# Kernel optimization log

Hardware: AMD Instinct MI355X
Metric: run time of the kernel (lower is better)

The kernel has to match this reference:

```python
import jax, jax.numpy as jnp
import numpy as np

B, S, C = 32, 1024, 12      # sentences, words per sentence, chars per word
E, H = 256, 512             # embedding dim, word-LSTM hidden dim
V, CS, T = 50000, 128, 50   # vocab, charset, tagset


def _lstm(x, Wih, Whh, b):
    """Standard torch LSTM (gate order i,f,g,o). x: [T, N, I] -> hidden trace [T, N, H]."""
    Hd = Whh.shape[1]
    N = x.shape[1]
    h0 = jnp.zeros((N, Hd), x.dtype)
    c0 = jnp.zeros((N, Hd), x.dtype)

    def step(carry, xt):
        h, c = carry
        gates = xt @ Wih.T + h @ Whh.T + b
        i, f, g, o = jnp.split(gates, 4, axis=-1)
        c = jax.nn.sigmoid(f) * c + jax.nn.sigmoid(i) * jnp.tanh(g)
        h = jax.nn.sigmoid(o) * jnp.tanh(c)
        return (h, c), h

    _, hs = jax.lax.scan(step, (h0, c0), x)
    return hs


def setup_inputs() -> dict:
    key = jax.random.key(0)
    ks = jax.random.split(key, 12)
    sc = 0.05
    return {
        "char_idx": jax.random.randint(ks[0], (B, S, C), 0, CS),
        "word_idx": jax.random.randint(ks[1], (B, S), 0, V),
        "char_emb": jax.random.normal(ks[2], (CS, E), jnp.float32) * sc,
        "word_emb": jax.random.normal(ks[3], (V, E), jnp.float32) * sc,
        "Wc_ih": jax.random.normal(ks[4], (4 * E, E), jnp.float32) * sc,
        "Wc_hh": jax.random.normal(ks[5], (4 * E, E), jnp.float32) * sc,
        "bc": jnp.zeros((4 * E,), jnp.float32),
        "Ww_ih": jax.random.normal(ks[6], (4 * H, 2 * E), jnp.float32) * sc,
        "Ww_hh": jax.random.normal(ks[7], (4 * H, H), jnp.float32) * sc,
        "bw": jnp.zeros((4 * H,), jnp.float32),
        "Wt": jax.random.normal(ks[8], (T, H), jnp.float32) * sc,
        "bt": jnp.zeros((T,), jnp.float32),
    }


def reference(char_idx, word_idx, char_emb, word_emb, Wc_ih, Wc_hh, bc,
              Ww_ih, Ww_hh, bw, Wt, bt):
    # --- character-level LSTM: each word starts from a fresh zero state ---
    ce = char_emb[char_idx]                       # [B, S, C, E]
    ce = ce.reshape(B * S, C, E).transpose(1, 0, 2)  # [C, B*S, E]
    char_hs = _lstm(ce, Wc_ih, Wc_hh, bc)         # [C, B*S, E]
    char_feat = char_hs[-1].reshape(B, S, E)      # last char output per word

    # --- word-level LSTM over concatenated [word_emb ; char_feat] ---
    we = word_emb[word_idx]                       # [B, S, E]
    x = jnp.concatenate([we, char_feat], axis=-1) # [B, S, 2E]
    x = x.transpose(1, 0, 2)                      # [S, B, 2E]
    word_hs = _lstm(x, Ww_ih, Ww_hh, bw)          # [S, B, H]
    word_hs = word_hs.transpose(1, 0, 2)          # [B, S, H]

    # --- tag projection + log_softmax per token ---
    logits = word_hs @ Wt.T + bt                  # [B, S, T]
    return jax.nn.log_softmax(logits, axis=-1)
```

## Files before the change

### kernel.cpp

```cpp
#include <hip/hip_runtime.h>
#include <stdint.h>
#include <stddef.h>

#define NB   32
#define NS   1024
#define NC   12
#define NE   256
#define NH   512
#define NT   50
#define NWRD 32768
#define MC   1024
#define RW   2048
#define KW   512

typedef short bf16x8 __attribute__((ext_vector_type(8)));
typedef short bf16x4 __attribute__((ext_vector_type(4)));
typedef float f32x4  __attribute__((ext_vector_type(4)));

#define MFMA16(a,b,c) __builtin_amdgcn_mfma_f32_16x16x32_bf16(a, b, c, 0, 0, 0)

__device__ __forceinline__ float bf2f(short u){
  return __uint_as_float(((uint32_t)(uint16_t)u) << 16);
}
__device__ __forceinline__ short f2bf(float f){
  uint32_t u = __float_as_uint(f);
  uint32_t r = (u + 0x7FFFu + ((u >> 16) & 1u)) >> 16;
  return (short)r;
}
__device__ __forceinline__ float sigf(float x){
  float e = __expf(-fabsf(x));
  float s = 1.0f / (1.0f + e);
  return x >= 0.0f ? s : 1.0f - s;
}
__device__ __forceinline__ float tanh_f(float x){
  float e = __expf(-2.0f * fabsf(x));
  float r = (1.0f - e) / (1.0f + e);
  return x >= 0.0f ? r : -r;
}

__global__ __launch_bounds__(256) void k_prep_pe(
    const float* __restrict__ char_emb, const float* __restrict__ Wc_ih,
    const float* __restrict__ bc, float* __restrict__ PEb)
{
  __shared__ float ce[NE];
  int a = blockIdx.x, tid = threadIdx.x;
  ce[tid] = char_emb[a * NE + tid];
  __syncthreads();
  int j = tid;
  float acc[4];
  #pragma unroll
  for (int g = 0; g < 4; ++g) acc[g] = 0.0f;
  for (int k = 0; k < NE; ++k) {
    float c = ce[k];
    #pragma unroll
    for (int g = 0; g < 4; ++g)
      acc[g] += c * Wc_ih[(size_t)(g * NE + j) * NE + k];
  }
  float4 o;
  o.x = acc[0] + bc[0 * NE + j];
  o.y = acc[1] + bc[1 * NE + j];
  o.z = acc[2] + bc[2 * NE + j];
  o.w = acc[3] + bc[3 * NE + j];
  *(float4*)&PEb[(size_t)a * MC + j * 4] = o;
}

__global__ __launch_bounds__(256) void k_prep_w(
    const float* __restrict__ Wc_hh, const float* __restrict__ Ww_ih,
    const float* __restrict__ Ww_hh, const float* __restrict__ bw,
    short* __restrict__ WhhC, short* __restrict__ WihW,
    short* __restrict__ WhhW, float* __restrict__ bwI)
{
  int r = blockIdx.x;
  int j = r >> 2, g = r & 3, tid = threadIdx.x;
  if (r < MC) {
    float v = Wc_hh[(size_t)(g * NE + j) * NE + tid];
    WhhC[(size_t)r * NE + tid] = f2bf(v);
  }
  #pragma unroll
  for (int kk = 0; kk < 2; ++kk) {
    int k = tid + kk * 256;
    WihW[(size_t)r * KW + k] = f2bf(Ww_ih[(size_t)(g * NH + j) * KW + k]);
    WhhW[(size_t)r * NH + k] = f2bf(Ww_hh[(size_t)(g * NH + j) * NH + k]);
  }
  if (tid == 0) bwI[r] = bw[g * NH + j];
}

__global__ __launch_bounds__(256) void k_char0(
    const int* __restrict__ char_idx, const float* __restrict__ PEb,
    float* __restrict__ c_state, short* __restrict__ h_out)
{
  int w = blockIdx.x, j = threadIdx.x;
  int idx = char_idx[w * NC + 0];
  float4 pe = *(const float4*)&PEb[(size_t)idx * MC + j * 4];
  float c = sigf(pe.x) * tanh_f(pe.z);
  float h = sigf(pe.w) * tanh_f(c);
  c_state[(size_t)w * NE + j] = c;
  h_out[(size_t)w * NE + j] = f2bf(h);
}

template<int KDIM, int EPI>
__global__ __launch_bounds__(256) void gemm_epi(
    const short* __restrict__ Amat, const short* __restrict__ Bmat,
    const float* __restrict__ PEb, const int* __restrict__ char_idx, int tstep,
    float* __restrict__ c_state, short* __restrict__ h_out,
    const float* __restrict__ bias, short* __restrict__ pw_out)
{
  __shared__ __align__(16) short As[128 * 64];
  __shared__ __align__(16) short Bs[128 * 64];
  const int tid = threadIdx.x;
  const int lane = tid & 63;
  const int wid = tid >> 6;
  const int wm = wid >> 1, wn = wid & 1;
  const int m0 = blockIdx.y * 128;
  const int n0 = blockIdx.x * 128;
  const int lo = lane & 15, hi = lane >> 4;

  f32x4 acc[4][4];
  #pragma unroll
  for (int i = 0; i < 4; ++i)
    #pragma unroll
    for (int j = 0; j < 4; ++j) acc[i][j] = (f32x4)0.0f;

  const int nk = KDIM / 64;
  for (int ki = 0; ki < nk; ++ki) {
    __syncthreads();
    #pragma unroll
    for (int it = 0; it < 4; ++it) {
      int cid = tid + it * 256;
      int row = cid >> 3, cp = cid & 7;
      int kch = cp ^ (row & 7);
      *(bf16x8*)&As[row * 64 + cp * 8] =
          *(const bf16x8*)&Amat[(size_t)(m0 + row) * KDIM + ki * 64 + kch * 8];
      *(bf16x8*)&Bs[row * 64 + cp * 8] =
          *(const bf16x8*)&Bmat[(size_t)(n0 + row) * KDIM + ki * 64 + kch * 8];
    }
    __syncthreads();
    #pragma unroll
    for (int kc = 0; kc < 2; ++kc) {
      bf16x8 af[4], bfr[4];
      #pragma unroll
      for (int fm = 0; fm < 4; ++fm) {
        int row = wm * 64 + fm * 16 + lo;
        int ch = (kc * 4 + hi) ^ (row & 7);
        af[fm] = *(bf16x8*)&As[row * 64 + ch * 8];
      }
      #pragma unroll
      for (int fn = 0; fn < 4; ++fn) {
        int row = wn * 64 + fn * 16 + lo;
        int ch = (kc * 4 + hi) ^ (row & 7);
        bfr[fn] = *(bf16x8*)&Bs[row * 64 + ch * 8];
      }
      #pragma unroll
      for (int fm = 0; fm < 4; ++fm)
        #pragma unroll
        for (int fn = 0; fn < 4; ++fn)
          acc[fm][fn] = MFMA16(af[fm], bfr[fn], acc[fm][fn]);
    }
  }

  #pragma unroll
  for (int fm = 0; fm < 4; ++fm) {
    int r0 = m0 + wm * 64 + fm * 16 + hi * 4;
    #pragma unroll
    for (int fn = 0; fn < 4; ++fn) {
      int w = n0 + wn * 64 + fn * 16 + lo;
      if constexpr (EPI == 0) {
        int idx = char_idx[w * NC + tstep];
        float4 pe = *(const float4*)&PEb[(size_t)idx * MC + r0];
        float gi = acc[fm][fn][0] + pe.x;
        float gf = acc[fm][fn][1] + pe.y;
        float gg = acc[fm][fn][2] + pe.z;
        float go = acc[fm][fn][3] + pe.w;
        int j = r0 >> 2;
        float c = sigf(gf) * c_state[(size_t)w * NE + j] + sigf(gi) * tanh_f(gg);
        c_state[(size_t)w * NE + j] = c;
        h_out[(size_t)w * NE + j] = f2bf(sigf(go) * tanh_f(c));
      } else {
        float4 bb = *(const float4*)&bias[r0];
        bf16x4 o;
        o[0] = f2bf(acc[fm][fn][0] + bb.x);
        o[1] = f2bf(acc[fm][fn][1] + bb.y);
        o[2] = f2bf(acc[fm][fn][2] + bb.z);
        o[3] = f2bf(acc[fm][fn][3] + bb.w);
        *(bf16x4*)&pw_out[(size_t)w * RW + r0] = o;
      }
    }
  }
}

__global__ __launch_bounds__(64) void k_xw(
    const int* __restrict__ word_idx, const float* __restrict__ word_emb,
    const short* __restrict__ h_char, short* __restrict__ Xw)
{
  int wp = blockIdx.x;
  int s = wp >> 5, b = wp & 31;
  int w = b * NS + s;
  int tid = threadIdx.x;
  int widx = word_idx[w];
  #pragma unroll
  for (int g = 0; g < 2; ++g) {
    int k4 = (tid + g * 64) * 4;
    bf16x4 o;
    if (k4 < NE) {
      float4 v = *(const float4*)&word_emb[(size_t)widx * NE + k4];
      o[0] = f2bf(v.x); o[1] = f2bf(v.y); o[2] = f2bf(v.z); o[3] = f2bf(v.w);
    } else {
      o = *(const bf16x4*)&h_char[(size_t)w * NE + (k4 - NE)];
    }
    *(bf16x4*)&Xw[(size_t)wp * KW + k4] = o;
  }
}

__global__ __launch_bounds__(512, 2) void k_word(
    const short* __restrict__ Whh,
    const short* __restrict__ PW,
    unsigned long long* __restrict__ hx64,
    short* __restrict__ word_hs)
{
  __shared__ __align__(16) short h_lds[2][32 * 520];
  const int tid = threadIdx.x, lane = tid & 63, wv = tid >> 6;
  const int lo = lane & 15, hi = lane >> 4;
  const int bk = blockIdx.x;
  const int wr = wv >> 1, wc = wv & 1;
  const int rowbase = bk * 64 + wr * 16;
  const int b = wc * 16 + lo;
  const int jl = (rowbase >> 2) + hi;
  const int r4 = rowbase + hi * 4;

  bf16x8 a[16];
  #pragma unroll
  for (int kc = 0; kc < 16; ++kc)
    a[kc] = *(const bf16x8*)&Whh[(size_t)(rowbase + lo) * NH + kc * 32 + hi * 8];

  float cst = 0.0f;
  bf16x4 pw = *(const bf16x4*)&PW[(size_t)(0 * NB + b) * RW + r4];

  const int jp_own = tid & 255;
  const int bgrp = tid >> 8;

  for (int s = 0; s < NS; ++s) {
    int sn = (s + 1 < NS) ? (s + 1) : (NS - 1);
    bf16x4 pwn = *(const bf16x4*)&PW[(size_t)(sn * NB + b) * RW + r4];

    const unsigned long long* src = hx64 + ((s & 1) << 13);
    unsigned long long v[16];
    #pragma unroll
    for (int i = 0; i < 16; ++i)
      v[i] = __hip_atomic_load(&src[i * 512 + tid], __ATOMIC_RELAXED, __HIP_MEMORY_SCOPE_AGENT);
    const unsigned int tv = (unsigned int)s;
    for (;;) {
      bool ok = true;
      #pragma unroll
      for (int i = 0; i < 16; ++i) {
        if ((unsigned int)(v[i] >> 32) != tv) {
          ok = false;
          v[i] = __hip_atomic_load(&src[i * 512 + tid], __ATOMIC_RELAXED, __HIP_MEMORY_SCOPE_AGENT);
        }
      }
      if (ok) break;
      __builtin_amdgcn_s_sleep(1);
    }

    short* buf = &h_lds[s & 1][0];
    #pragma unroll
    for (int i = 0; i < 16; ++i) {
      int bb = 2 * i + bgrp;
      *(unsigned int*)&buf[bb * 520 + 2 * jp_own] = (unsigned int)v[i];
    }
    __syncthreads();

    f32x4 acc;
    #pragma unroll
    for (int q = 0; q < 4; ++q) acc[q] = bf2f(pw[q]);
    #pragma unroll
    for (int kc = 0; kc < 16; ++kc) {
      bf16x8 hb = *(bf16x8*)((const char*)buf + b * 1040 + kc * 64 + hi * 16);
      acc = MFMA16(a[kc], hb, acc);
    }

    float c = sigf(acc[1]) * cst + sigf(acc[0]) * tanh_f(acc[2]);
    cst = c;
    short hv = f2bf(sigf(acc[3]) * tanh_f(c));

    unsigned int own = (unsigned int)(unsigned short)hv;
    unsigned int part = (unsigned int)__shfl_xor((int)own, 16);
    if ((hi & 1) == 0) {
      unsigned long long val = (((unsigned long long)(unsigned int)(s + 1)) << 32)
                             | ((unsigned long long)part << 16) | (unsigned long long)own;
      __hip_atomic_store(&hx64[(((s + 1) & 1) << 13) + (b << 8) + (jl >> 1)], val,
                         __ATOMIC_RELAXED, __HIP_MEMORY_SCOPE_AGENT);
    }
    word_hs[((size_t)b * NS + s) * NH + jl] = hv;
    pw = pwn;
  }
}

__global__ __launch_bounds__(256) void k_tags(
    const short* __restrict__ word_hs, const float* __restrict__ Wt,
    const float* __restrict__ bt, float* __restrict__ out)
{
  __shared__ __align__(16) short Ws[64 * 256];
  const int tid = threadIdx.x, lane = tid & 63, wid = tid >> 6;
  const int lo = lane & 15, hi = lane >> 4;
  const int n0 = blockIdx.x * 128;
  const int wb = n0 + wid * 32;

  f32x4 acc[4][2];
  #pragma unroll
  for (int fm = 0; fm < 4; ++fm)
    #pragma unroll
    for (int fn = 0; fn < 2; ++fn) acc[fm][fn] = (f32x4)0.0f;

  for (int half = 0; half < 2; ++half) {
    __syncthreads();
    for (int cid = tid; cid < 2048; cid += 256) {
      int row = cid >> 5, cp = cid & 31;
      int kch = cp ^ (row & 7);
      bf16x8 v;
      if (row < NT) {
        const float* src = &Wt[(size_t)row * KW + half * 256 + kch * 8];
        #pragma unroll
        for (int e = 0; e < 8; ++e) v[e] = f2bf(src[e]);
      } else v = (bf16x8)0;
      *(bf16x8*)&Ws[row * 256 + cp * 8] = v;
    }
    __syncthreads();
    #pragma unroll
    for (int kc = 0; kc < 8; ++kc) {
      bf16x8 bfr[2];
      #pragma unroll
      for (int fn = 0; fn < 2; ++fn) {
        int w = wb + fn * 16 + lo;
        bfr[fn] = *(const bf16x8*)&word_hs[(size_t)w * KW + half * 256 + kc * 32 + hi * 8];
      }
      #pragma unroll
      for (int fm = 0; fm < 4; ++fm) {
        int row = fm * 16 + lo;
        int ch = (kc * 4 + hi) ^ (row & 7);
        bf16x8 av = *(bf16x8*)&Ws[row * 256 + ch * 8];
        acc[fm][0] = MFMA16(av, bfr[0], acc[fm][0]);
        acc[fm][1] = MFMA16(av, bfr[1], acc[fm][1]);
      }
    }
  }

  #pragma unroll
  for (int fn = 0; fn < 2; ++fn) {
    int w = wb + fn * 16 + lo;
    float lg[16];
    float m = -1e30f;
    #pragma unroll
    for (int fm = 0; fm < 4; ++fm)
      #pragma unroll
      for (int q = 0; q < 4; ++q) {
        int tg = fm * 16 + hi * 4 + q;
        float bv = (tg < NT) ? bt[tg] : 0.0f;
        float v = acc[fm][fn][q] + bv;
        lg[fm * 4 + q] = v;
        if (tg < NT) m = fmaxf(m, v);
      }
    m = fmaxf(m, __shfl_xor(m, 16));
    m = fmaxf(m, __shfl_xor(m, 32));
    float s = 0.0f;
    #pragma unroll
    for (int fm = 0; fm < 4; ++fm)
      #pragma unroll
      for (int q = 0; q < 4; ++q) {
        int tg = fm * 16 + hi * 4 + q;
        if (tg < NT) s += __expf(lg[fm * 4 + q] - m);
      }
    s += __shfl_xor(s, 16);
    s += __shfl_xor(s, 32);
    float lz = m + __logf(s);
    #pragma unroll
    for (int fm = 0; fm < 4; ++fm)
      #pragma unroll
      for (int q = 0; q < 4; ++q) {
        int tg = fm * 16 + hi * 4 + q;
        if (tg < NT) out[(size_t)w * NT + tg] = lg[fm * 4 + q] - lz;
      }
  }
}

extern "C" void kernel_launch(void* const* d_in, const int* in_sizes, int n_in,
                              void* d_out, int out_size, void* d_ws, size_t ws_size,
                              hipStream_t stream) {
  const int*   char_idx = (const int*)  d_in[0];
  const int*   word_idx = (const int*)  d_in[1];
  const float* char_emb = (const float*)d_in[2];
  const float* word_emb = (const float*)d_in[3];
  const float* Wc_ih    = (const float*)d_in[4];
  const float* Wc_hh    = (const float*)d_in[5];
  const float* bc       = (const float*)d_in[6];
  const float* Ww_ih    = (const float*)d_in[7];
  const float* Ww_hh    = (const float*)d_in[8];
  const float* bw       = (const float*)d_in[9];
  const float* Wt       = (const float*)d_in[10];
  const float* bt       = (const float*)d_in[11];
  float* out = (float*)d_out;

  const size_t MB = 1ull << 20;
  uint8_t* w8 = (uint8_t*)d_ws;
  float* PEb   = (float*)(w8 + 0);
  short* WhhC  = (short*)(w8 + 512 * 1024);
  short* WihW  = (short*)(w8 + 1 * MB);
  short* WhhW  = (short*)(w8 + 3 * MB);
  float* bwI   = (float*)(w8 + 5 * MB);
  unsigned long long* hx64 = (unsigned long long*)(w8 + 5 * MB + 64 * 1024);
  short* hA    = (short*)(w8 + 6 * MB);
  short* hB    = (short*)(w8 + 22 * MB);
  short* whs   = (short*)(w8 + 6 * MB);
  float* cC    = (float*)(w8 + 38 * MB);
  short* Xw    = (short*)(w8 + 38 * MB);
  short* PW    = (short*)(w8 + 70 * MB);

  k_prep_pe<<<128, 256, 0, stream>>>(char_emb, Wc_ih, bc, PEb);
  k_prep_w<<<2048, 256, 0, stream>>>(Wc_hh, Ww_ih, Ww_hh, bw, WhhC, WihW, WhhW, bwI);

  k_char0<<<NWRD, 256, 0, stream>>>(char_idx, PEb, cC, hA);
  for (int t = 1; t < NC; ++t) {
    short* src = (t & 1) ? hA : hB;
    short* dst = (t & 1) ? hB : hA;
    gemm_epi<256, 0><<<dim3(256, 8), 256, 0, stream>>>(
        WhhC, src, PEb, char_idx, t, cC, dst, nullptr, nullptr);
  }

  k_xw<<<NWRD, 64, 0, stream>>>(word_idx, word_emb, hB, Xw);
  gemm_epi<512, 1><<<dim3(256, 16), 256, 0, stream>>>(
      WihW, Xw, nullptr, nullptr, 0, nullptr, nullptr, bwI, PW);

  hipMemsetAsync(hx64, 0, 128 * 1024, stream);
  k_word<<<32, 512, 0, stream>>>(WhhW, PW, hx64, whs);

  k_tags<<<256, 256, 0, stream>>>(whs, Wt, bt, out);
}
```

Measured before the change: 4.632 ms.

## Replace tagged 64-bit h exchange with data plus per-wave flag protocol in word LSTM

The word-LSTM cross-block exchange no longer packs a step tag into every 64-bit hidden-state word. Each wave now stores plain bf16 pairs, waits for its stores to drain, then publishes a per-wave step flag. Consumers poll 256 flags with one vectorized sc1 load and a ballot, then bulk-load the hidden state in 16-byte chunks. This halves exchange traffic and reduces per-thread polling work, but adds a store-drain wait and relies on sc1 cache semantics for ordering. Separately, the MFMA chain is split into four independent accumulators to shorten the dependency chain.

After: 4.423 ms. 1.05x faster.

```diff
diff --git a/kernel.cpp b/kernel.cpp
--- a/kernel.cpp
+++ b/kernel.cpp
@@ -16,6 +16,7 @@
 typedef short bf16x8 __attribute__((ext_vector_type(8)));
 typedef short bf16x4 __attribute__((ext_vector_type(4)));
 typedef float f32x4  __attribute__((ext_vector_type(4)));
+typedef unsigned int u32x4 __attribute__((ext_vector_type(4)));
 
 #define MFMA16(a,b,c) __builtin_amdgcn_mfma_f32_16x16x32_bf16(a, b, c, 0, 0, 0)
 
@@ -214,7 +215,7 @@
 __global__ __launch_bounds__(512, 2) void k_word(
     const short* __restrict__ Whh,
     const short* __restrict__ PW,
-    unsigned long long* __restrict__ hx64,
+    uint8_t* __restrict__ xb,
     short* __restrict__ word_hs)
 {
   __shared__ __align__(16) short h_lds[2][32 * 520];
@@ -232,51 +233,84 @@
   for (int kc = 0; kc < 16; ++kc)
     a[kc] = *(const bf16x8*)&Whh[(size_t)(rowbase + lo) * NH + kc * 32 + hi * 8];
 
+  short*    hdat  = (short*)xb;
+  uint32_t* flags = (uint32_t*)(xb + 65536);
+
+  const int db = tid >> 4, dlo = (tid & 15) * 8;
+  const short* dA = hdat + db * 512 + dlo;
+  const short* dB = dA + 16384;
+  const uint32_t* fA = flags + lane * 4;
+  const uint32_t* fB = fA + 256;
+
   float cst = 0.0f;
-  bf16x4 pw = *(const bf16x4*)&PW[(size_t)(0 * NB + b) * RW + r4];
-
-  const int jp_own = tid & 255;
-  const int bgrp = tid >> 8;
+  bf16x4 pw = *(const bf16x4*)&PW[(size_t)b * RW + r4];
 
   for (int s = 0; s < NS; ++s) {
+    const uint32_t tv = (uint32_t)s;
+    const int par = s & 1;
+
     int sn = (s + 1 < NS) ? (s + 1) : (NS - 1);
     bf16x4 pwn = *(const bf16x4*)&PW[(size_t)(sn * NB + b) * RW + r4];
 
-    const unsigned long long* src = hx64 + ((s & 1) << 13);
-    unsigned long long v[16];
-    #pragma unroll
-    for (int i = 0; i < 16; ++i)
-      v[i] = __hip_atomic_load(&src[i * 512 + tid], __ATOMIC_RELAXED, __HIP_MEMORY_SCOPE_AGENT);
-    const unsigned int tv = (unsigned int)s;
-    for (;;) {
-      bool ok = true;
-      #pragma unroll
-      for (int i = 0; i < 16; ++i) {
-        if ((unsigned int)(v[i] >> 32) != tv) {
-          ok = false;
-          v[i] = __hip_atomic_load(&src[i * 512 + tid], __ATOMIC_RELAXED, __HIP_MEMORY_SCOPE_AGENT);
+    {
+      const uint32_t* fp = par ? fB : fA;
+      int tries = 0;
+      for (;;) {
+        u32x4 f;
+        asm volatile("global_load_dwordx4 %0, %1, off sc1\n\t"
+                     "s_waitcnt vmcnt(0)"
+                     : "=v"(f) : "v"(fp));
+        bool ok = (f[0] == tv) & (f[1] == tv) & (f[2] == tv) & (f[3] == tv);
+        if (__ballot(ok) == ~0ull) break;
+        if (++tries > 768) {
+          uint32_t g0 = __hip_atomic_load(fp + 0, __ATOMIC_RELAXED, __HIP_MEMORY_SCOPE_AGENT);
+          uint32_t g1 = __hip_atomic_load(fp + 1, __ATOMIC_RELAXED, __HIP_MEMORY_SCOPE_AGENT);
+          uint32_t g2 = __hip_atomic_load(fp + 2, __ATOMIC_RELAXED, __HIP_MEMORY_SCOPE_AGENT);
+          uint32_t g3 = __hip_atomic_load(fp + 3, __ATOMIC_RELAXED, __HIP_MEMORY_SCOPE_AGENT);
+          bool ok2 = (g0 == tv) & (g1 == tv) & (g2 == tv) & (g3 == tv);
+          if (__ballot(ok2) == ~0ull) break;
+          tries = 0;
         }
-      }
-      if (ok) break;
-      __builtin_amdgcn_s_sleep(1);
-    }
-
-    short* buf = &h_lds[s & 1][0];
-    #pragma unroll
-    for (int i = 0; i < 16; ++i) {
-      int bb = 2 * i + bgrp;
-      *(unsigned int*)&buf[bb * 520 + 2 * jp_own] = (unsigned int)v[i];
-    }
+        __builtin_amdgcn_s_sleep(1);
+      }
+    }
+
+    const short* sp = par ? dB : dA;
+    bf16x8 d0, d1, d2, d3;
+    asm volatile("global_load_dwordx4 %0, %4, off sc1\n\t"
+                 "global_load_dwordx4 %1, %4, off offset:256 sc1\n\t"
+                 "global_load_dwordx4 %2, %4, off offset:512 sc1\n\t"
+                 "global_load_dwordx4 %3, %4, off offset:768 sc1\n\t"
+                 "s_waitcnt vmcnt(0)"
+                 : "=v"(d0), "=v"(d1), "=v"(d2), "=v"(d3) : "v"(sp));
+
+    short* buf = &h_lds[par][0];
+    short* dst = buf + db * 520 + dlo;
+    *(bf16x8*)&dst[0]   = d0;
+    *(bf16x8*)&dst[128] = d1;
+    *(bf16x8*)&dst[256] = d2;
+    *(bf16x8*)&dst[384] = d3;
     __syncthreads();
 
+    f32x4 acc0, acc1, acc2, acc3;
+    #pragma unroll
+    for (int q = 0; q < 4; ++q) {
+      acc0[q] = bf2f(pw[q]); acc1[q] = 0.0f; acc2[q] = 0.0f; acc3[q] = 0.0f;
+    }
+    #pragma unroll
+    for (int kc = 0; kc < 16; kc += 4) {
+      bf16x8 h0 = *(bf16x8*)((const char*)buf + b * 1040 + (kc + 0) * 64 + hi * 16);
+      bf16x8 h1 = *(bf16x8*)((const char*)buf + b * 1040 + (kc + 1) * 64 + hi * 16);
+      bf16x8 h2 = *(bf16x8*)((const char*)buf + b * 1040 + (kc + 2) * 64 + hi * 16);
+      bf16x8 h3 = *(bf16x8*)((const char*)buf + b * 1040 + (kc + 3) * 64 + hi * 16);
+      acc0 = MFMA16(a[kc + 0], h0, acc0);
+      acc1 = MFMA16(a[kc + 1], h1, acc1);
+      acc2 = MFMA16(a[kc + 2], h2, acc2);
+      acc3 = MFMA16(a[kc + 3], h3, acc3);
+    }
     f32x4 acc;
     #pragma unroll
-    for (int q = 0; q < 4; ++q) acc[q] = bf2f(pw[q]);
-    #pragma unroll
-    for (int kc = 0; kc < 16; ++kc) {
-      bf16x8 hb = *(bf16x8*)((const char*)buf + b * 1040 + kc * 64 + hi * 16);
-      acc = MFMA16(a[kc], hb, acc);
-    }
+    for (int q = 0; q < 4; ++q) acc[q] = (acc0[q] + acc1[q]) + (acc2[q] + acc3[q]);
 
     float c = sigf(acc[1]) * cst + sigf(acc[0]) * tanh_f(acc[2]);
     cst = c;
@@ -284,11 +318,17 @@
 
     unsigned int own = (unsigned int)(unsigned short)hv;
     unsigned int part = (unsigned int)__shfl_xor((int)own, 16);
+    const int npar = (s + 1) & 1;
     if ((hi & 1) == 0) {
-      unsigned long long val = (((unsigned long long)(unsigned int)(s + 1)) << 32)
-                             | ((unsigned long long)part << 16) | (unsigned long long)own;
-      __hip_atomic_store(&hx64[(((s + 1) & 1) << 13) + (b << 8) + (jl >> 1)], val,
-                         __ATOMIC_RELAXED, __HIP_MEMORY_SCOPE_AGENT);
+      unsigned int val = own | (part << 16);
+      short* hp = hdat + (npar << 14) + b * 512 + jl;
+      asm volatile("global_store_dword %0, %1, off sc1" :: "v"(hp), "v"(val) : "memory");
+    }
+    asm volatile("s_waitcnt vmcnt(0)" ::: "memory");
+    if (lane == 0) {
+      uint32_t* fq = flags + npar * 256 + bk * 8 + wv;
+      asm volatile("global_store_dword %0, %1, off sc1"
+                   :: "v"(fq), "v"((uint32_t)(s + 1)) : "memory");
     }
     word_hs[((size_t)b * NS + s) * NH + jl] = hv;
     pw = pwn;
@@ -406,7 +446,7 @@
   short* WihW  = (short*)(w8 + 1 * MB);
   short* WhhW  = (short*)(w8 + 3 * MB);
   float* bwI   = (float*)(w8 + 5 * MB);
-  unsigned long long* hx64 = (unsigned long long*)(w8 + 5 * MB + 64 * 1024);
+  uint8_t* xb  = (uint8_t*)(w8 + 5 * MB + 64 * 1024);
   short* hA    = (short*)(w8 + 6 * MB);
   short* hB    = (short*)(w8 + 22 * MB);
   short* whs   = (short*)(w8 + 6 * MB);
@@ -429,8 +469,8 @@
   gemm_epi<512, 1><<<dim3(256, 16), 256, 0, stream>>>(
       WihW, Xw, nullptr, nullptr, 0, nullptr, nullptr, bwI, PW);
 
-  hipMemsetAsync(hx64, 0, 128 * 1024, stream);
-  k_word<<<32, 512, 0, stream>>>(WhhW, PW, hx64, whs);
+  hipMemsetAsync(xb, 0, 64 * 1024 + 2048, stream);
+  k_word<<<32, 512, 0, stream>>>(WhhW, PW, xb, whs);
 
   k_tags<<<256, 256, 0, stream>>>(whs, Wt, bt, out);
 }
```

## Repack word-LSTM cross-block handoff as tagged 32-bit words with vector polling

Applied to the files above, without the earlier changes.

The cross-block exchange of hidden state in the persistent word-LSTM kernel is reworked. Each thread now publishes a single 32-bit word (16-bit step tag plus bf16 value) instead of shuffling lanes to form 64-bit tagged pairs. Consumers poll with inline-asm dwordx4 loads carrying sc1 cache bits, re-fetching only stale chunks. The change also splits the MFMA accumulation into four independent chains, prefetches the input projection two steps ahead, and drops the min-blocks launch bound. The aim is lower per-step synchronization latency on the serial 1024-step path, at the cost of relying on hand-written memory ordering and cache-bit semantics for correctness.

Result: slower. 7.079 ms (+52.8%).

```diff
diff --git a/kernel.cpp b/kernel.cpp
--- a/kernel.cpp
+++ b/kernel.cpp
@@ -16,6 +16,8 @@
 typedef short bf16x8 __attribute__((ext_vector_type(8)));
 typedef short bf16x4 __attribute__((ext_vector_type(4)));
 typedef float f32x4  __attribute__((ext_vector_type(4)));
+typedef unsigned int u32x2 __attribute__((ext_vector_type(2)));
+typedef unsigned int u32x4 __attribute__((ext_vector_type(4)));
 
 #define MFMA16(a,b,c) __builtin_amdgcn_mfma_f32_16x16x32_bf16(a, b, c, 0, 0, 0)
 
@@ -211,10 +213,10 @@
   }
 }
 
-__global__ __launch_bounds__(512, 2) void k_word(
+__global__ __launch_bounds__(512) void k_word(
     const short* __restrict__ Whh,
     const short* __restrict__ PW,
-    unsigned long long* __restrict__ hx64,
+    uint32_t* __restrict__ hx,
     short* __restrict__ word_hs)
 {
   __shared__ __align__(16) short h_lds[2][32 * 520];
@@ -232,66 +234,104 @@
   for (int kc = 0; kc < 16; ++kc)
     a[kc] = *(const bf16x8*)&Whh[(size_t)(rowbase + lo) * NH + kc * 32 + hi * 8];
 
+  const int db = tid >> 4, q0 = (tid & 15) * 4;
+  const uint32_t* pA = hx + db * 512 + q0;
+  const uint32_t* pB = pA + 16384;
+
   float cst = 0.0f;
-  bf16x4 pw = *(const bf16x4*)&PW[(size_t)(0 * NB + b) * RW + r4];
-
-  const int jp_own = tid & 255;
-  const int bgrp = tid >> 8;
+  bf16x4 pw  = *(const bf16x4*)&PW[(size_t)(0 * NB + b) * RW + r4];
+  bf16x4 pw1 = *(const bf16x4*)&PW[(size_t)(1 * NB + b) * RW + r4];
 
   for (int s = 0; s < NS; ++s) {
-    int sn = (s + 1 < NS) ? (s + 1) : (NS - 1);
-    bf16x4 pwn = *(const bf16x4*)&PW[(size_t)(sn * NB + b) * RW + r4];
-
-    const unsigned long long* src = hx64 + ((s & 1) << 13);
-    unsigned long long v[16];
-    #pragma unroll
-    for (int i = 0; i < 16; ++i)
-      v[i] = __hip_atomic_load(&src[i * 512 + tid], __ATOMIC_RELAXED, __HIP_MEMORY_SCOPE_AGENT);
-    const unsigned int tv = (unsigned int)s;
-    for (;;) {
-      bool ok = true;
-      #pragma unroll
-      for (int i = 0; i < 16; ++i) {
-        if ((unsigned int)(v[i] >> 32) != tv) {
-          ok = false;
-          v[i] = __hip_atomic_load(&src[i * 512 + tid], __ATOMIC_RELAXED, __HIP_MEMORY_SCOPE_AGENT);
-        }
-      }
-      if (ok) break;
-      __builtin_amdgcn_s_sleep(1);
-    }
-
-    short* buf = &h_lds[s & 1][0];
-    #pragma unroll
-    for (int i = 0; i < 16; ++i) {
-      int bb = 2 * i + bgrp;
-      *(unsigned int*)&buf[bb * 520 + 2 * jp_own] = (unsigned int)v[i];
+    const int par = s & 1;
+    const uint32_t tvs = (uint32_t)s << 16;
+
+    const uint32_t* sp = par ? pB : pA;
+    u32x4 v0, v1, v2, v3, v4, v5, v6, v7;
+    asm volatile(
+        "global_load_dwordx4 %0, %8, off sc1\n\t"
+        "global_load_dwordx4 %1, %8, off offset:256 sc1\n\t"
+        "global_load_dwordx4 %2, %8, off offset:512 sc1\n\t"
+        "global_load_dwordx4 %3, %8, off offset:768 sc1\n\t"
+        "global_load_dwordx4 %4, %8, off offset:1024 sc1\n\t"
+        "global_load_dwordx4 %5, %8, off offset:1280 sc1\n\t"
+        "global_load_dwordx4 %6, %8, off offset:1536 sc1\n\t"
+        "global_load_dwordx4 %7, %8, off offset:1792 sc1\n\t"
+        "s_waitcnt vmcnt(0)"
+        : "=&v"(v0), "=&v"(v1), "=&v"(v2), "=&v"(v3),
+          "=&v"(v4), "=&v"(v5), "=&v"(v6), "=&v"(v7)
+        : "v"(sp));
+    u32x4 vv[8] = {v0, v1, v2, v3, v4, v5, v6, v7};
+    uint32_t bad;
+    {
+      auto chk = [&](const u32x4& c) -> uint32_t {
+        uint32_t x = (c[0] ^ tvs) | (c[1] ^ tvs) | (c[2] ^ tvs) | (c[3] ^ tvs);
+        return (x >> 16) != 0u;
+      };
+      bad = 0;
+      #pragma unroll
+      for (int k = 0; k < 8; ++k) bad |= chk(vv[k]) << k;
+      while (bad) {
+        #pragma unroll
+        for (int k = 0; k < 8; ++k)
+          if (bad & (1u << k)) {
+            u32x4 r;
+            asm volatile("global_load_dwordx4 %0, %1, off sc1\n\t"
+                         "s_waitcnt vmcnt(0)"
+                         : "=&v"(r) : "v"(sp + k * 64));
+            vv[k] = r;
+          }
+        bad = 0;
+        #pragma unroll
+        for (int k = 0; k < 8; ++k) bad |= chk(vv[k]) << k;
+      }
+    }
+
+    int s2 = (s + 2 < NS) ? (s + 2) : (NS - 1);
+    bf16x4 pw2 = *(const bf16x4*)&PW[(size_t)(s2 * NB + b) * RW + r4];
+
+    uint32_t* buf32 = (uint32_t*)&h_lds[par][0];
+    #pragma unroll
+    for (int k = 0; k < 8; ++k) {
+      uint32_t p0 = (vv[k][0] & 0xFFFFu) | (vv[k][1] << 16);
+      uint32_t p1 = (vv[k][2] & 0xFFFFu) | (vv[k][3] << 16);
+      u32x2 pr; pr[0] = p0; pr[1] = p1;
+      *(u32x2*)&buf32[db * 260 + k * 32 + (q0 >> 1)] = pr;
     }
     __syncthreads();
 
+    const short* buf = &h_lds[par][0];
+    f32x4 acc0, acc1, acc2, acc3;
+    #pragma unroll
+    for (int q = 0; q < 4; ++q) {
+      acc0[q] = bf2f(pw[q]); acc1[q] = 0.0f; acc2[q] = 0.0f; acc3[q] = 0.0f;
+    }
+    #pragma unroll
+    for (int kc = 0; kc < 16; kc += 4) {
+      bf16x8 h0 = *(bf16x8*)((const char*)buf + b * 1040 + (kc + 0) * 64 + hi * 16);
+      bf16x8 h1 = *(bf16x8*)((const char*)buf + b * 1040 + (kc + 1) * 64 + hi * 16);
+      bf16x8 h2 = *(bf16x8*)((const char*)buf + b * 1040 + (kc + 2) * 64 + hi * 16);
+      bf16x8 h3 = *(bf16x8*)((const char*)buf + b * 1040 + (kc + 3) * 64 + hi * 16);
+      acc0 = MFMA16(a[kc + 0], h0, acc0);
+      acc1 = MFMA16(a[kc + 1], h1, acc1);
+      acc2 = MFMA16(a[kc + 2], h2, acc2);
+      acc3 = MFMA16(a[kc + 3], h3, acc3);
+    }
     f32x4 acc;
     #pragma unroll
-    for (int q = 0; q < 4; ++q) acc[q] = bf2f(pw[q]);
-    #pragma unroll
-    for (int kc = 0; kc < 16; ++kc) {
-      bf16x8 hb = *(bf16x8*)((const char*)buf + b * 1040 + kc * 64 + hi * 16);
-      acc = MFMA16(a[kc], hb, acc);
-    }
+    for (int q = 0; q < 4; ++q) acc[q] = (acc0[q] + acc1[q]) + (acc2[q] + acc3[q]);
 
     float c = sigf(acc[1]) * cst + sigf(acc[0]) * tanh_f(acc[2]);
     cst = c;
     short hv = f2bf(sigf(acc[3]) * tanh_f(c));
 
-    unsigned int own = (unsigned int)(unsigned short)hv;
-    unsigned int part = (unsigned int)__shfl_xor((int)own, 16);
-    if ((hi & 1) == 0) {
-      unsigned long long val = (((unsigned long long)(unsigned int)(s + 1)) << 32)
-                             | ((unsigned long long)part << 16) | (unsigned long long)own;
-      __hip_atomic_store(&hx64[(((s + 1) & 1) << 13) + (b << 8) + (jl >> 1)], val,
-                         __ATOMIC_RELAXED, __HIP_MEMORY_SCOPE_AGENT);
+    {
+      uint32_t pub = ((uint32_t)(s + 1) << 16) | (uint32_t)(uint16_t)hv;
+      uint32_t* hp = hx + (((s + 1) & 1) << 14) + b * 512 + jl;
+      asm volatile("global_store_dword %0, %1, off sc1" :: "v"(hp), "v"(pub) : "memory");
     }
     word_hs[((size_t)b * NS + s) * NH + jl] = hv;
-    pw = pwn;
+    pw = pw1; pw1 = pw2;
   }
 }
 
@@ -406,7 +446,7 @@
   short* WihW  = (short*)(w8 + 1 * MB);
   short* WhhW  = (short*)(w8 + 3 * MB);
   float* bwI   = (float*)(w8 + 5 * MB);
-  unsigned long long* hx64 = (unsigned long long*)(w8 + 5 * MB + 64 * 1024);
+  uint32_t* hx = (uint32_t*)(w8 + 5 * MB + 64 * 1024);
   short* hA    = (short*)(w8 + 6 * MB);
   short* hB    = (short*)(w8 + 22 * MB);
   short* whs   = (short*)(w8 + 6 * MB);
@@ -429,8 +469,8 @@
   gemm_epi<512, 1><<<dim3(256, 16), 256, 0, stream>>>(
       WihW, Xw, nullptr, nullptr, 0, nullptr, nullptr, bwI, PW);
 
-  hipMemsetAsync(hx64, 0, 128 * 1024, stream);
-  k_word<<<32, 512, 0, stream>>>(WhhW, PW, hx64, whs);
+  hipMemsetAsync(hx, 0, 128 * 1024, stream);
+  k_word<<<32, 512, 0, stream>>>(WhhW, PW, hx, whs);
 
   k_tags<<<256, 256, 0, stream>>>(whs, Wt, bt, out);
 }
```
